# Kernel optimization log

Measured on AMD Instinct MI355X. Metric: run time of the kernel, lower is better.

The kernel has to match this reference:

```python
import jax, jax.numpy as jnp
import numpy as np
from jax import lax

V, EMB, ENH, DNH, ZD, K = 51, 64, 256, 256, 32, 512
B, T = 1024, 128


def gru_scan(xs, h0, Wih, Whh, bih, bhh, collect):
    """PyTorch-convention GRU. xs: [T,B,D], h0: [B,H]. Returns (ys or None, hT)."""
    def step(h, x):
        gi = x @ Wih.T + bih          # [B, 3H]
        gh = h @ Whh.T + bhh          # [B, 3H]
        ir, iz, inn = jnp.split(gi, 3, axis=-1)
        hr, hz, hn = jnp.split(gh, 3, axis=-1)
        r = jax.nn.sigmoid(ir + hr)
        zg = jax.nn.sigmoid(iz + hz)
        n = jnp.tanh(inn + r * hn)
        hnew = (1.0 - zg) * n + zg * h
        return hnew, (hnew if collect else None)
    hT, ys = lax.scan(step, h0, xs)
    return ys, hT


def setup_inputs() -> dict:
    key = jax.random.key(0)
    ks = jax.random.split(key, 24)
    w = lambda k, shape, s=0.1: (jax.random.normal(k, shape, jnp.float32) * s)
    inp = {
        "x": jax.random.randint(ks[0], (B, T), 0, V),
        "emb_enc": w(ks[1], (V, EMB)),
        "emb_dec": w(ks[2], (V, EMB)),
        # encoder bidirectional GRU (fwd + bwd directions)
        "Wih_f": w(ks[3], (3 * ENH, EMB)), "Whh_f": w(ks[4], (3 * ENH, ENH)),
        "bih_f": w(ks[5], (3 * ENH,)), "bhh_f": w(ks[6], (3 * ENH,)),
        "Wih_b": w(ks[7], (3 * ENH, EMB)), "Whh_b": w(ks[8], (3 * ENH, ENH)),
        "bih_b": w(ks[9], (3 * ENH,)), "bhh_b": w(ks[10], (3 * ENH,)),
        # down_to_z: Linear(2*ENC_NH -> Z_NH)
        "Wdown": w(ks[11], (ZD, 2 * ENH)), "bdown": w(ks[12], (ZD,)),
        # VQ codebook, uniform(-1/K, 1/K) as in source
        "codebook": jax.random.uniform(ks[13], (K, ZD), jnp.float32, -1.0 / K, 1.0 / K),
        # up_from_z: Linear(Z_NH -> DEC_NH)
        "Wup": w(ks[14], (DNH, ZD)), "bup": w(ks[15], (DNH,)),
        # decoder GRU: input = INPUT_EMB_DIM + Z_NH
        "Wih_d": w(ks[16], (3 * DNH, EMB + ZD)), "Whh_d": w(ks[17], (3 * DNH, DNH)),
        "bih_d": w(ks[18], (3 * DNH,)), "bhh_d": w(ks[19], (3 * DNH,)),
        # output projection Linear(DEC_NH -> VOCABSIZE)
        "Wout": w(ks[20], (V, DNH)), "bout": w(ks[21], (V,)),
    }
    return inp


def reference(x, emb_enc, emb_dec, Wih_f, Whh_f, bih_f, bhh_f,
              Wih_b, Whh_b, bih_b, bhh_b, Wdown, bdown, codebook,
              Wup, bup, Wih_d, Whh_d, bih_d, bhh_d, Wout, bout):
    sg = lax.stop_gradient
    Bsz, Tlen = x.shape

    # ---- Encoder: bidirectional GRU, keep final hidden of each direction ----
    e = emb_enc[x]                              # [B,T,EMB]
    xs = jnp.transpose(e, (1, 0, 2))            # [T,B,EMB]
    h0 = jnp.zeros((Bsz, ENH), e.dtype)
    _, hf = gru_scan(xs, h0, Wih_f, Whh_f, bih_f, bhh_f, collect=False)
    _, hb = gru_scan(xs[::-1], h0, Wih_b, Whh_b, bih_b, bhh_b, collect=False)
    out_h = jnp.concatenate([hf, hb], axis=-1)  # [B, 2*ENH]

    # ---- down to z ----
    z = out_h @ Wdown.T + bdown                 # [B, ZD]

    # ---- VQ quantizer ----
    d2 = (z ** 2).sum(-1, keepdims=True) + (codebook ** 2).sum(-1) - 2.0 * (z @ codebook.T)  # [B,K]
    idx = jnp.argmin(d2, axis=-1)               # [B]
    quantized = codebook[idx]                   # [B, ZD]
    commit = ((sg(quantized) - z) ** 2).mean(-1)
    embed_l = ((quantized - sg(z)) ** 2).mean(-1)
    qloss = 0.1 * commit + 0.1 * embed_l
    Q = jnp.sum(qloss)
    qz = z + sg(quantized - z)                  # straight-through [B, ZD]

    # ---- up to decoder hidden ----
    hidden = qz @ Wup.T + bup                   # [B, DNH]

    # ---- Decoder GRU over src, z concatenated at every step ----
    src, tgt = x[:, :-1], x[:, 1:]
    d = emb_dec[src]                            # [B,T-1,EMB]
    zrep = jnp.broadcast_to(qz[:, None, :], (Bsz, Tlen - 1, ZD))
    dec_in = jnp.concatenate([zrep, d], axis=-1)            # [B,T-1,EMB+ZD]
    ys, _ = gru_scan(jnp.transpose(dec_in, (1, 0, 2)), hidden,
                     Wih_d, Whh_d, bih_d, bhh_d, collect=True)  # [T-1,B,DNH]
    logits = jnp.transpose(ys, (1, 0, 2)) @ Wout.T + bout   # [B,T-1,V]

    # cross entropy, reduction='sum', ignore_index=0
    logp = jax.nn.log_softmax(logits, axis=-1)
    nll = -jnp.take_along_axis(logp, tgt[..., None], axis=-1).squeeze(-1)  # [B,T-1]
    mask = (tgt != 0)
    xloss = jnp.sum(nll * mask)
    nonpadded_tokens = jnp.sum(mask)
    pred_tokens = jnp.argmax(logits, axis=-1)

    return (xloss, nonpadded_tokens, pred_tokens, Q, idx[:, None])
```

## Files before the change

kernel.cpp:

```cpp
#include <hip/hip_runtime.h>
#include <cstdint>

typedef unsigned short u16;
typedef unsigned int u32;
typedef __attribute__((ext_vector_type(4))) int int4v;
typedef __attribute__((ext_vector_type(8))) short short8;
typedef __attribute__((ext_vector_type(4))) float f32x4;

#define XLOSS_OFF 0
#define NPAD_OFF  1
#define PRED_OFF  2
#define Q_OFF     130050
#define IDX_OFF   130051

__device__ __forceinline__ u16 f2b(float f){
  union { float f; unsigned int i; } c; c.f = f;
  unsigned int i = c.i;
  unsigned int r = (i + 0x7FFFu + ((i >> 16) & 1u)) >> 16;
  return (u16)r;
}

#define LOG2E 1.442695040889634f
__device__ __forceinline__ float fast_sigmoid(float x){
  return __builtin_amdgcn_rcpf(1.f + __builtin_amdgcn_exp2f(-LOG2E*x));
}
__device__ __forceinline__ float fast_tanh(float x){
  return 1.f - 2.f*__builtin_amdgcn_rcpf(1.f + __builtin_amdgcn_exp2f((2.f*LOG2E)*x));
}

__global__ __launch_bounds__(256) void k_prep_wo(
    const float* __restrict__ Wo, u16* __restrict__ oWo, float* __restrict__ dout){
  int idx = blockIdx.x*256 + threadIdx.x;
  if (idx == 0){ dout[XLOSS_OFF]=0.f; dout[NPAD_OFF]=0.f; dout[Q_OFF]=0.f; }
  int row = idx >> 8, k = idx & 255;
  oWo[idx] = (row < 51) ? f2b(Wo[row*256 + k]) : (u16)0;
}

__global__ __launch_bounds__(64) void k_prep_q(
    const float* __restrict__ Wf, const float* __restrict__ Wb, const float* __restrict__ Wd,
    signed char* __restrict__ qf, signed char* __restrict__ qb, signed char* __restrict__ qd,
    float* __restrict__ invf, float* __restrict__ invb, float* __restrict__ invd){
  const int row = blockIdx.x;
  const int mat = row / 768, r = row - mat*768;
  const float* W = (mat==0 ? Wf : (mat==1 ? Wb : Wd)) + (size_t)r*256;
  signed char* q = (mat==0 ? qf : (mat==1 ? qb : qd)) + (size_t)r*256;
  float* inv     = (mat==0 ? invf : (mat==1 ? invb : invd));
  const int lane = threadIdx.x;
  float4 v = *(const float4*)(W + lane*4);
  float m = fmaxf(fmaxf(fabsf(v.x),fabsf(v.y)), fmaxf(fabsf(v.z),fabsf(v.w)));
  #pragma unroll
  for (int off=32; off>0; off>>=1) m = fmaxf(m, __shfl_xor(m, off));
  m = fmaxf(m, 1e-20f);
  const float s = 127.f / m;
  int a0 = __float2int_rn(v.x*s), a1 = __float2int_rn(v.y*s);
  int a2 = __float2int_rn(v.z*s), a3 = __float2int_rn(v.w*s);
  u32 packed = (a0&255) | ((a1&255)<<8) | ((a2&255)<<16) | ((a3&255)<<24);
  *(u32*)(q + lane*4) = packed;
  if (lane == 0) inv[r] = m * (1.f/127.f);
}

__global__ __launch_bounds__(256) void k_prep_g(
    const float* __restrict__ emb_e, const float* __restrict__ emb_d,
    const float* __restrict__ Wih_f, const float* __restrict__ bih_f, const float* __restrict__ bhh_f,
    const float* __restrict__ Wih_b, const float* __restrict__ bih_b, const float* __restrict__ bhh_b,
    const float* __restrict__ Wih_d,
    float* __restrict__ Gf, float* __restrict__ Gb, float* __restrict__ Gd){
  int idx = blockIdx.x*256 + threadIdx.x;
  int tab = idx / 39168;
  int rem = idx - tab*39168;
  int v = rem / 768;
  int n = rem - v*768;
  float acc = 0.f;
  if (tab == 0){
    const float* e = emb_e + v*64; const float* w = Wih_f + n*64;
    for (int k=0;k<64;k++) acc += e[k]*w[k];
    acc += bih_f[n] + (n < 512 ? bhh_f[n] : 0.f);
    Gf[rem] = acc;
  } else if (tab == 1){
    const float* e = emb_e + v*64; const float* w = Wih_b + n*64;
    for (int k=0;k<64;k++) acc += e[k]*w[k];
    acc += bih_b[n] + (n < 512 ? bhh_b[n] : 0.f);
    Gb[rem] = acc;
  } else {
    const float* e = emb_d + v*64; const float* w = Wih_d + n*96 + 32;
    for (int k=0;k<64;k++) acc += e[k]*w[k];
    Gd[rem] = acc;
  }
}

template<int MODE>
__global__ __launch_bounds__(1024)
__attribute__((amdgpu_waves_per_eu(4, 4)))
void k_gru(
    const signed char* __restrict__ W0, const signed char* __restrict__ W1,
    const float* __restrict__ I0, const float* __restrict__ I1,
    const float* __restrict__ G0, const float* __restrict__ G1,
    const float* __restrict__ bhh0, const float* __restrict__ bhh1,
    const int* __restrict__ x,
    const float* __restrict__ zc, const float* __restrict__ h0g,
    float* __restrict__ out_h, u16* __restrict__ ys){
  const int tid = threadIdx.x;
  const int lane = tid & 63;
  const int wave = tid >> 6;
  const int l15 = lane & 15, lhi = lane >> 4;

  bool fwd = true; int gb;
  const signed char* W; const float* G; const float* bhh; const float* invS;
  if (MODE == 0){
    int bi = blockIdx.x;
    fwd = bi < 64; gb = fwd ? bi : bi - 64;
    W = fwd ? W0 : W1; G = fwd ? G0 : G1; bhh = fwd ? bhh0 : bhh1;
    invS = fwd ? I0 : I1;
  } else {
    gb = blockIdx.x; W = W0; G = G0; bhh = bhh0; invS = I0;
  }
  const int b0 = gb * 16;
  const int nT = (MODE == 0) ? 128 : 127;
  const float HS    = (MODE == 0) ? 127.f : 63.f;
  const float invHS = (MODE == 0) ? (1.f/127.f) : (1.f/63.f);

  __shared__ signed char hbf[2*4096];
  __shared__ int xsh[2048];
  __shared__ float zcs[(MODE==1) ? (16*768) : 4];

  const int c = wave*16 + l15;

  int4v wq0[4], wq1[4], wq2[4];
  {
    const signed char* p0 = W + (size_t)(c      )*256 + lhi*16;
    const signed char* p1 = W + (size_t)(c + 256)*256 + lhi*16;
    const signed char* p2 = W + (size_t)(c + 512)*256 + lhi*16;
    #pragma unroll
    for (int kt=0; kt<4; kt++){
      wq0[kt] = *(const int4v*)(p0 + kt*64);
      wq1[kt] = *(const int4v*)(p1 + kt*64);
      wq2[kt] = *(const int4v*)(p2 + kt*64);
    }
  }
  #pragma unroll
  for (int kt=0; kt<4; kt++){
    asm volatile("" : "+v"(wq0[kt]));
    asm volatile("" : "+v"(wq1[kt]));
    asm volatile("" : "+v"(wq2[kt]));
  }
  const float isr = invS[c]       * invHS;
  const float isz = invS[256 + c] * invHS;
  const float isn = invS[512 + c] * invHS;
  const float bnv = bhh[512 + c];

  for (int i = tid; i < 2048; i += 1024) xsh[i] = x[b0*128 + i];
  if (MODE == 1){
    for (int i = tid; i < 12288; i += 1024) zcs[i] = zc[(size_t)b0*768 + i];
  }

  float hreg[4];
  #pragma unroll
  for (int r=0;r<4;r++){
    const int m = 4*lhi + r;
    float hv = (MODE==0) ? 0.f : h0g[(size_t)(b0+m)*256 + c];
    hreg[r] = hv;
    int hq = __float2int_rn(fminf(fmaxf(hv*HS, -127.f), 127.f));
    hbf[m*256 + (c ^ ((m&15)<<4))] = (signed char)hq;
  }
  __syncthreads();

  int aoff[4];
  #pragma unroll
  for (int kt=0; kt<4; kt++)
    aoff[kt] = l15*256 + ((kt*64 + lhi*16) ^ (l15<<4));

  int cur = 0;
  for (int t=0; t<nT; ++t){
    const signed char* hb = hbf + (cur<<12);
    int4v af[4];
    #pragma unroll
    for (int kt=0; kt<4; kt++) af[kt] = *(const int4v*)(hb + aoff[kt]);

    int4v acc0 = {0,0,0,0}, acc1 = {0,0,0,0}, acc2 = {0,0,0,0};
    #pragma unroll
    for (int kt=0; kt<4; kt++){
      acc0 = __builtin_amdgcn_mfma_i32_16x16x64_i8(af[kt], wq0[kt], acc0, 0,0,0);
      acc1 = __builtin_amdgcn_mfma_i32_16x16x64_i8(af[kt], wq1[kt], acc1, 0,0,0);
      acc2 = __builtin_amdgcn_mfma_i32_16x16x64_i8(af[kt], wq2[kt], acc2, 0,0,0);
    }

    const int te = (MODE==0 && !fwd) ? (127 - t) : t;
    signed char* nbuf = hbf + ((cur^1)<<12);
    #pragma unroll
    for (int r=0;r<4;r++){
      const int m = 4*lhi + r;
      const int tok = xsh[(m<<7) + te];
      const float* Gp = G + (size_t)tok*768;
      float gr = Gp[c], gz = Gp[256 + c], gn = Gp[512 + c];
      if (MODE==1){
        const float* zp = &zcs[m*768];
        gr += zp[c]; gz += zp[256 + c]; gn += zp[512 + c];
      }
      float ghr = (float)acc0[r] * isr;
      float ghz = (float)acc1[r] * isz;
      float ghn = (float)acc2[r] * isn;
      float rg = fast_sigmoid(ghr + gr);
      float zg = fast_sigmoid(ghz + gz);
      float nn = fast_tanh(gn + rg*(ghn + bnv));
      float hv = nn + zg*(hreg[r] - nn);
      hreg[r] = hv;
      int hq = __float2int_rn(fminf(fmaxf(hv*HS, -127.f), 127.f));
      nbuf[m*256 + (c ^ ((m&15)<<4))] = (signed char)hq;
      if (MODE == 1){
        ys[((size_t)(b0+m)*127 + t)*256 + c] = f2b(hv);
      }
    }
    __syncthreads();
    cur ^= 1;
  }

  if (MODE == 0){
    #pragma unroll
    for (int r=0;r<4;r++){
      const int m = 4*lhi + r;
      out_h[(size_t)(b0+m)*512 + (fwd ? 0 : 256) + c] = hreg[r];
    }
  }
}

__global__ __launch_bounds__(64) void k_vq(
    const float* __restrict__ outH, const float* __restrict__ Wdown, const float* __restrict__ bdown,
    const float* __restrict__ cb, const float* __restrict__ Wup, const float* __restrict__ bup,
    const float* __restrict__ Wihd, const float* __restrict__ bihd, const float* __restrict__ bhhd,
    float* __restrict__ hidden, float* __restrict__ zc, float* __restrict__ dout){
  const int b = blockIdx.x;
  const int lane = threadIdx.x;
  __shared__ float oh[512];
  __shared__ float zsh[32];
  __shared__ float qsh[32];
  {
    const float* src = outH + (size_t)b*512 + lane*8;
    *(float4*)&oh[lane*8]   = *(const float4*)src;
    *(float4*)&oh[lane*8+4] = *(const float4*)(src+4);
  }
  __syncthreads();
  if (lane < 32){
    float acc = bdown[lane];
    const float* wr = Wdown + lane*512;
    for (int k=0;k<512;k++) acc += wr[k]*oh[k];
    zsh[lane] = acc;
  }
  __syncthreads();
  float bd = 3.4e38f; int bi = 0;
  for (int c8=0;c8<8;c8++){
    const int c = lane*8 + c8;
    const float* cr = cb + c*32;
    float d = 0.f;
    #pragma unroll
    for (int k=0;k<32;k++){ float df = zsh[k]-cr[k]; d += df*df; }
    if (d < bd){ bd = d; bi = c; }
  }
  #pragma unroll
  for (int offm=32; offm>0; offm>>=1){
    float od = __shfl_xor(bd, offm);
    int   oi = __shfl_xor(bi, offm);
    if (od < bd || (od == bd && oi < bi)){ bd = od; bi = oi; }
  }
  if (lane == 0){
    atomicAdd(&dout[Q_OFF], bd * (0.2f/32.f));
    dout[IDX_OFF + b] = (float)bi;
  }
  if (lane < 32) qsh[lane] = cb[(size_t)bi*32 + lane];
  __syncthreads();
  #pragma unroll
  for (int i=0;i<4;i++){
    const int o = lane*4 + i;
    float acc = bup[o];
    const float* wr = Wup + o*32;
    #pragma unroll
    for (int k=0;k<32;k++) acc += wr[k]*qsh[k];
    hidden[(size_t)b*256 + o] = acc;
  }
  #pragma unroll
  for (int i=0;i<12;i++){
    const int o = lane*12 + i;
    float acc = bihd[o] + (o < 512 ? bhhd[o] : 0.f);
    const float* wr = Wihd + (size_t)o*96;
    #pragma unroll
    for (int k=0;k<32;k++) acc += wr[k]*qsh[k];
    zc[(size_t)b*768 + o] = acc;
  }
}

__global__ __launch_bounds__(256) void k_out(
    const u16* __restrict__ ys, const u16* __restrict__ Wo,
    const float* __restrict__ bout, const int* __restrict__ x,
    float* __restrict__ dout){
  const int tid = threadIdx.x;
  const int w = tid >> 6, lane = tid & 63;
  const int l15 = lane & 15, lhi = lane >> 4;
  __shared__ float lg[4][32][66];
  const int rows0 = blockIdx.x*128 + w*32;
  const f32x4 fz = {0.f,0.f,0.f,0.f};
  #pragma unroll
  for (int mt=0; mt<2; mt++){
    const int rb = rows0 + mt*16;
    f32x4 acc[4];
    #pragma unroll
    for (int nt=0;nt<4;nt++) acc[nt] = fz;
    #pragma unroll
    for (int kt=0; kt<8; kt++){
      short8 a = *(const short8*)&ys[(size_t)(rb + l15)*256 + kt*32 + lhi*8];
      #pragma unroll
      for (int nt=0; nt<4; nt++){
        short8 bb = *(const short8*)&Wo[(size_t)(nt*16 + l15)*256 + kt*32 + lhi*8];
        acc[nt] = __builtin_amdgcn_mfma_f32_16x16x32_bf16(a, bb, acc[nt], 0, 0, 0);
      }
    }
    #pragma unroll
    for (int nt=0;nt<4;nt++){
      const int col = nt*16 + l15;
      const float bo = (col < 51) ? bout[col] : 0.f;
      #pragma unroll
      for (int r=0;r<4;r++){
        float v = (col < 51) ? (acc[nt][r] + bo) : -1e30f;
        lg[w][mt*16 + lhi*4 + r][col] = v;
      }
    }
  }
  __syncthreads();
  float xl = 0.f, ct = 0.f;
  if (lane < 32){
    const int grow = rows0 + lane;
    const float* Lr = &lg[w][lane][0];
    float m = Lr[0]; int am = 0;
    for (int i=1;i<51;i++){ float v = Lr[i]; if (v > m){ m = v; am = i; } }
    float s = 0.f;
    for (int i=0;i<51;i++) s += __expf(Lr[i] - m);
    const int bb = grow / 127;
    const int tt = grow - bb*127;
    const int tgt = x[bb*128 + tt + 1];
    const float nll = (m + __logf(s)) - Lr[tgt];
    const float mk = (tgt != 0) ? 1.f : 0.f;
    dout[PRED_OFF + grow] = (float)am;
    xl = nll * mk; ct = mk;
  }
  #pragma unroll
  for (int off=32; off>0; off>>=1){
    xl += __shfl_xor(xl, off);
    ct += __shfl_xor(ct, off);
  }
  if (lane == 0){
    atomicAdd(&dout[XLOSS_OFF], xl);
    atomicAdd(&dout[NPAD_OFF], ct);
  }
}

extern "C" void kernel_launch(void* const* d_in, const int* in_sizes, int n_in,
                              void* d_out, int out_size, void* d_ws, size_t ws_size,
                              hipStream_t stream){
  (void)in_sizes; (void)n_in; (void)out_size; (void)ws_size;
  const int*   x      = (const int*)  d_in[0];
  const float* emb_e  = (const float*)d_in[1];
  const float* emb_d  = (const float*)d_in[2];
  const float* Wih_f  = (const float*)d_in[3];
  const float* Whh_f  = (const float*)d_in[4];
  const float* bih_f  = (const float*)d_in[5];
  const float* bhh_f  = (const float*)d_in[6];
  const float* Wih_b  = (const float*)d_in[7];
  const float* Whh_b  = (const float*)d_in[8];
  const float* bih_b  = (const float*)d_in[9];
  const float* bhh_b  = (const float*)d_in[10];
  const float* Wdown  = (const float*)d_in[11];
  const float* bdown  = (const float*)d_in[12];
  const float* cbook  = (const float*)d_in[13];
  const float* Wup    = (const float*)d_in[14];
  const float* bup    = (const float*)d_in[15];
  const float* Wih_d  = (const float*)d_in[16];
  const float* Whh_d  = (const float*)d_in[17];
  const float* bih_d  = (const float*)d_in[18];
  const float* bhh_d  = (const float*)d_in[19];
  const float* Wout   = (const float*)d_in[20];
  const float* bout   = (const float*)d_in[21];
  float* dout = (float*)d_out;

  char* ws = (char*)d_ws;
  size_t off = 0;
  auto nxt = [&](size_t bytes)->char*{
    char* r = ws + off;
    off += (bytes + 255) & ~(size_t)255;
    return r;
  };
  signed char* Wq_f = (signed char*)nxt((size_t)196608);
  signed char* Wq_b = (signed char*)nxt((size_t)196608);
  signed char* Wq_d = (signed char*)nxt((size_t)196608);
  float* invF = (float*)nxt((size_t)768*4);
  float* invB = (float*)nxt((size_t)768*4);
  float* invD = (float*)nxt((size_t)768*4);
  float* Gf    = (float*)nxt((size_t)39168*4);
  float* Gb    = (float*)nxt((size_t)39168*4);
  float* Gd    = (float*)nxt((size_t)39168*4);
  u16*   Wo_bf = (u16*)  nxt((size_t)16384*2);
  float* outH  = (float*)nxt((size_t)524288*4);
  float* hid   = (float*)nxt((size_t)262144*4);
  float* zcw   = (float*)nxt((size_t)786432*4);
  u16*   ysb   = (u16*)  nxt((size_t)33292288*2);

  hipLaunchKernelGGL(k_prep_wo, dim3(64), dim3(256), 0, stream, Wout, Wo_bf, dout);
  hipLaunchKernelGGL(k_prep_q, dim3(2304), dim3(64), 0, stream,
                     Whh_f, Whh_b, Whh_d, Wq_f, Wq_b, Wq_d, invF, invB, invD);
  hipLaunchKernelGGL(k_prep_g, dim3(459), dim3(256), 0, stream,
                     emb_e, emb_d, Wih_f, bih_f, bhh_f, Wih_b, bih_b, bhh_b, Wih_d,
                     Gf, Gb, Gd);
  hipLaunchKernelGGL((k_gru<0>), dim3(128), dim3(1024), 0, stream,
                     Wq_f, Wq_b, invF, invB, Gf, Gb, bhh_f, bhh_b, x,
                     (const float*)nullptr, (const float*)nullptr, outH, (u16*)nullptr);
  hipLaunchKernelGGL(k_vq, dim3(1024), dim3(64), 0, stream,
                     outH, Wdown, bdown, cbook, Wup, bup, Wih_d, bih_d, bhh_d,
                     hid, zcw, dout);
  hipLaunchKernelGGL((k_gru<1>), dim3(64), dim3(1024), 0, stream,
                     Wq_d, (const signed char*)nullptr, invD, (const float*)nullptr,
                     Gd, (const float*)nullptr, bhh_d, (const float*)nullptr, x,
                     zcw, hid, (float*)nullptr, ysb);
  hipLaunchKernelGGL(k_out, dim3(1016), dim3(256), 0, stream,
                     ysb, Wo_bf, bout, x, dout);
}
```

Measured before the change: 578.1 us.

## Stage r/z recurrent weights in LDS instead of registers in GRU kernel

The r and z gate int8 recurrent weights move from per-thread registers into a swizzled 128KB LDS buffer that is loaded once per block. Only the n-gate weights stay register-resident. Each step now reads the r/z weight fragments from LDS alongside the hidden state, which frees VGPRs but adds LDS traffic to every recurrence step. The decoder's per-batch z contribution is read directly from global memory instead of staged in LDS, and dynamic shared memory of 144KB is requested for both GRU launches.

```diff
diff --git a/kernel.cpp b/kernel.cpp
--- a/kernel.cpp
+++ b/kernel.cpp
@@ -12,6 +12,8 @@
 #define PRED_OFF  2
 #define Q_OFF     130050
 #define IDX_OFF   130051
+
+#define GRU_LDS_BYTES 147456
 
 __device__ __forceinline__ u16 f2b(float f){
   union { float f; unsigned int i; } c; c.f = f;
@@ -99,6 +101,11 @@
     const int* __restrict__ x,
     const float* __restrict__ zc, const float* __restrict__ h0g,
     float* __restrict__ out_h, u16* __restrict__ ys){
+  extern __shared__ char smem[];
+  signed char* wlds = (signed char*)smem;
+  signed char* hbf  = (signed char*)(smem + 131072);
+  int*         xsh  = (int*)(smem + 139264);
+
   const int tid = threadIdx.x;
   const int lane = tid & 63;
   const int wave = tid >> 6;
@@ -119,39 +126,32 @@
   const float HS    = (MODE == 0) ? 127.f : 63.f;
   const float invHS = (MODE == 0) ? (1.f/127.f) : (1.f/63.f);
 
-  __shared__ signed char hbf[2*4096];
-  __shared__ int xsh[2048];
-  __shared__ float zcs[(MODE==1) ? (16*768) : 4];
-
   const int c = wave*16 + l15;
 
-  int4v wq0[4], wq1[4], wq2[4];
+  #pragma unroll
+  for (int it=0; it<8; ++it){
+    int i = tid + it*1024;
+    int row = i >> 4;
+    int ck  = (i & 15) << 4;
+    int4v v = *(const int4v*)(W + (size_t)row*256 + ck);
+    *(int4v*)(wlds + row*256 + (ck ^ ((row&15)<<4))) = v;
+  }
+
+  int4v wq2[4];
   {
-    const signed char* p0 = W + (size_t)(c      )*256 + lhi*16;
-    const signed char* p1 = W + (size_t)(c + 256)*256 + lhi*16;
     const signed char* p2 = W + (size_t)(c + 512)*256 + lhi*16;
     #pragma unroll
-    for (int kt=0; kt<4; kt++){
-      wq0[kt] = *(const int4v*)(p0 + kt*64);
-      wq1[kt] = *(const int4v*)(p1 + kt*64);
-      wq2[kt] = *(const int4v*)(p2 + kt*64);
-    }
-  }
-  #pragma unroll
-  for (int kt=0; kt<4; kt++){
-    asm volatile("" : "+v"(wq0[kt]));
-    asm volatile("" : "+v"(wq1[kt]));
-    asm volatile("" : "+v"(wq2[kt]));
-  }
+    for (int kt=0; kt<4; kt++) wq2[kt] = *(const int4v*)(p2 + kt*64);
+  }
+  #pragma unroll
+  for (int kt=0; kt<4; kt++){ asm volatile("" : "+v"(wq2[kt])); }
+
   const float isr = invS[c]       * invHS;
   const float isz = invS[256 + c] * invHS;
   const float isn = invS[512 + c] * invHS;
   const float bnv = bhh[512 + c];
 
   for (int i = tid; i < 2048; i += 1024) xsh[i] = x[b0*128 + i];
-  if (MODE == 1){
-    for (int i = tid; i < 12288; i += 1024) zcs[i] = zc[(size_t)b0*768 + i];
-  }
 
   float hreg[4];
   #pragma unroll
@@ -164,24 +164,25 @@
   }
   __syncthreads();
 
-  int aoff[4];
-  #pragma unroll
-  for (int kt=0; kt<4; kt++)
-    aoff[kt] = l15*256 + ((kt*64 + lhi*16) ^ (l15<<4));
+  int koff[4];
+  #pragma unroll
+  for (int kt=0; kt<4; kt++) koff[kt] = (kt*64 + lhi*16) ^ (l15<<4);
+  const int arow = l15 << 8;
+  const int wrow = (wave*16 + l15) << 8;
 
   int cur = 0;
   for (int t=0; t<nT; ++t){
     const signed char* hb = hbf + (cur<<12);
-    int4v af[4];
-    #pragma unroll
-    for (int kt=0; kt<4; kt++) af[kt] = *(const int4v*)(hb + aoff[kt]);
 
     int4v acc0 = {0,0,0,0}, acc1 = {0,0,0,0}, acc2 = {0,0,0,0};
     #pragma unroll
     for (int kt=0; kt<4; kt++){
-      acc0 = __builtin_amdgcn_mfma_i32_16x16x64_i8(af[kt], wq0[kt], acc0, 0,0,0);
-      acc1 = __builtin_amdgcn_mfma_i32_16x16x64_i8(af[kt], wq1[kt], acc1, 0,0,0);
-      acc2 = __builtin_amdgcn_mfma_i32_16x16x64_i8(af[kt], wq2[kt], acc2, 0,0,0);
+      int4v af = *(const int4v*)(hb + arow + koff[kt]);
+      int4v wr = *(const int4v*)(wlds + wrow + koff[kt]);
+      int4v wz = *(const int4v*)(wlds + wrow + 65536 + koff[kt]);
+      acc0 = __builtin_amdgcn_mfma_i32_16x16x64_i8(af, wr, acc0, 0,0,0);
+      acc1 = __builtin_amdgcn_mfma_i32_16x16x64_i8(af, wz, acc1, 0,0,0);
+      acc2 = __builtin_amdgcn_mfma_i32_16x16x64_i8(af, wq2[kt], acc2, 0,0,0);
     }
 
     const int te = (MODE==0 && !fwd) ? (127 - t) : t;
@@ -193,8 +194,8 @@
       const float* Gp = G + (size_t)tok*768;
       float gr = Gp[c], gz = Gp[256 + c], gn = Gp[512 + c];
       if (MODE==1){
-        const float* zp = &zcs[m*768];
-        gr += zp[c]; gz += zp[256 + c]; gn += zp[512 + c];
+        const float* zp = zc + (size_t)(b0+m)*768 + c;
+        gr += zp[0]; gz += zp[256]; gn += zp[512];
       }
       float ghr = (float)acc0[r] * isr;
       float ghz = (float)acc1[r] * isz;
@@ -401,19 +402,24 @@
   float* zcw   = (float*)nxt((size_t)786432*4);
   u16*   ysb   = (u16*)  nxt((size_t)33292288*2);
 
+  hipFuncSetAttribute((const void*)&k_gru<0>,
+                      hipFuncAttributeMaxDynamicSharedMemorySize, GRU_LDS_BYTES);
+  hipFuncSetAttribute((const void*)&k_gru<1>,
+                      hipFuncAttributeMaxDynamicSharedMemorySize, GRU_LDS_BYTES);
+
   hipLaunchKernelGGL(k_prep_wo, dim3(64), dim3(256), 0, stream, Wout, Wo_bf, dout);
   hipLaunchKernelGGL(k_prep_q, dim3(2304), dim3(64), 0, stream,
                      Whh_f, Whh_b, Whh_d, Wq_f, Wq_b, Wq_d, invF, invB, invD);
   hipLaunchKernelGGL(k_prep_g, dim3(459), dim3(256), 0, stream,
                      emb_e, emb_d, Wih_f, bih_f, bhh_f, Wih_b, bih_b, bhh_b, Wih_d,
                      Gf, Gb, Gd);
-  hipLaunchKernelGGL((k_gru<0>), dim3(128), dim3(1024), 0, stream,
+  hipLaunchKernelGGL((k_gru<0>), dim3(128), dim3(1024), GRU_LDS_BYTES, stream,
                      Wq_f, Wq_b, invF, invB, Gf, Gb, bhh_f, bhh_b, x,
                      (const float*)nullptr, (const float*)nullptr, outH, (u16*)nullptr);
   hipLaunchKernelGGL(k_vq, dim3(1024), dim3(64), 0, stream,
                      outH, Wdown, bdown, cbook, Wup, bup, Wih_d, bih_d, bhh_d,
                      hid, zcw, dout);
-  hipLaunchKernelGGL((k_gru<1>), dim3(64), dim3(1024), 0, stream,
+  hipLaunchKernelGGL((k_gru<1>), dim3(64), dim3(1024), GRU_LDS_BYTES, stream,
                      Wq_d, (const signed char*)nullptr, invD, (const float*)nullptr,
                      Gd, (const float*)nullptr, bhh_d, (const float*)nullptr, x,
                      zcw, hid, (float*)nullptr, ysb);
```

Result: slower. 628.4 us (+8.7%).

## Split GRU recurrence into 8-row blocks of 4 waves with register-held weights

Applied to the files above, without the earlier changes.

The recurrent GRU kernel goes from 1024-thread blocks over 16 batch rows to 256-thread blocks over 8 batch rows. This doubles the grid to 256 blocks for the encoder and 128 for the decoder, so more CUs run the serial time loop. Each wave now keeps 64 columns of all three gate weights in registers and issues 48 int8 MFMAs per step, and only half the lanes do the gate math because the M dimension is half used. Gate inputs are prefetched before the MFMAs, z-conditioning is held in registers, and decoder outputs are staged in shared memory for 16-byte coalesced stores at the cost of an extra barrier per step.

```diff
diff --git a/kernel.cpp b/kernel.cpp
--- a/kernel.cpp
+++ b/kernel.cpp
@@ -5,6 +5,7 @@
 typedef unsigned int u32;
 typedef __attribute__((ext_vector_type(4))) int int4v;
 typedef __attribute__((ext_vector_type(8))) short short8;
+typedef __attribute__((ext_vector_type(8))) unsigned short u16x8;
 typedef __attribute__((ext_vector_type(4))) float f32x4;
 
 #define XLOSS_OFF 0
@@ -89,8 +90,8 @@
 }
 
 template<int MODE>
-__global__ __launch_bounds__(1024)
-__attribute__((amdgpu_waves_per_eu(4, 4)))
+__global__ __launch_bounds__(256)
+__attribute__((amdgpu_waves_per_eu(1, 1)))
 void k_gru(
     const signed char* __restrict__ W0, const signed char* __restrict__ W1,
     const float* __restrict__ I0, const float* __restrict__ I1,
@@ -99,6 +100,10 @@
     const int* __restrict__ x,
     const float* __restrict__ zc, const float* __restrict__ h0g,
     float* __restrict__ out_h, u16* __restrict__ ys){
+  __shared__ signed char hbf[2*4096];
+  __shared__ int xsh[1024];
+  __shared__ u16 ysh[(MODE==1) ? 2048 : 4];
+
   const int tid = threadIdx.x;
   const int lane = tid & 63;
   const int wave = tid >> 6;
@@ -108,59 +113,80 @@
   const signed char* W; const float* G; const float* bhh; const float* invS;
   if (MODE == 0){
     int bi = blockIdx.x;
-    fwd = bi < 64; gb = fwd ? bi : bi - 64;
+    fwd = bi < 128; gb = fwd ? bi : bi - 128;
     W = fwd ? W0 : W1; G = fwd ? G0 : G1; bhh = fwd ? bhh0 : bhh1;
     invS = fwd ? I0 : I1;
   } else {
     gb = blockIdx.x; W = W0; G = G0; bhh = bhh0; invS = I0;
   }
-  const int b0 = gb * 16;
+  const int b0 = gb * 8;
   const int nT = (MODE == 0) ? 128 : 127;
   const float HS    = (MODE == 0) ? 127.f : 63.f;
   const float invHS = (MODE == 0) ? (1.f/127.f) : (1.f/63.f);
 
-  __shared__ signed char hbf[2*4096];
-  __shared__ int xsh[2048];
-  __shared__ float zcs[(MODE==1) ? (16*768) : 4];
-
-  const int c = wave*16 + l15;
-
-  int4v wq0[4], wq1[4], wq2[4];
-  {
-    const signed char* p0 = W + (size_t)(c      )*256 + lhi*16;
-    const signed char* p1 = W + (size_t)(c + 256)*256 + lhi*16;
-    const signed char* p2 = W + (size_t)(c + 512)*256 + lhi*16;
-    #pragma unroll
-    for (int kt=0; kt<4; kt++){
-      wq0[kt] = *(const int4v*)(p0 + kt*64);
-      wq1[kt] = *(const int4v*)(p1 + kt*64);
-      wq2[kt] = *(const int4v*)(p2 + kt*64);
-    }
-  }
-  #pragma unroll
-  for (int kt=0; kt<4; kt++){
-    asm volatile("" : "+v"(wq0[kt]));
-    asm volatile("" : "+v"(wq1[kt]));
-    asm volatile("" : "+v"(wq2[kt]));
-  }
-  const float isr = invS[c]       * invHS;
-  const float isz = invS[256 + c] * invHS;
-  const float isn = invS[512 + c] * invHS;
-  const float bnv = bhh[512 + c];
-
-  for (int i = tid; i < 2048; i += 1024) xsh[i] = x[b0*128 + i];
-  if (MODE == 1){
-    for (int i = tid; i < 12288; i += 1024) zcs[i] = zc[(size_t)b0*768 + i];
-  }
-
-  float hreg[4];
-  #pragma unroll
-  for (int r=0;r<4;r++){
-    const int m = 4*lhi + r;
-    float hv = (MODE==0) ? 0.f : h0g[(size_t)(b0+m)*256 + c];
-    hreg[r] = hv;
-    int hq = __float2int_rn(fminf(fmaxf(hv*HS, -127.f), 127.f));
-    hbf[m*256 + (c ^ ((m&15)<<4))] = (signed char)hq;
+  int4v wq[3][4][4];
+  #pragma unroll
+  for (int g=0; g<3; g++){
+    #pragma unroll
+    for (int ct=0; ct<4; ct++){
+      const signed char* p = W + (size_t)(g*256 + wave*64 + ct*16 + l15)*256 + lhi*16;
+      #pragma unroll
+      for (int kt=0; kt<4; kt++)
+        wq[g][ct][kt] = *(const int4v*)(p + kt*64);
+    }
+  }
+  #pragma unroll
+  for (int g=0; g<3; g++)
+    #pragma unroll
+    for (int ct=0; ct<4; ct++)
+      #pragma unroll
+      for (int kt=0; kt<4; kt++){ asm volatile("" : "+v"(wq[g][ct][kt])); }
+
+  float is_[3][4], bn_[4];
+  #pragma unroll
+  for (int ct=0; ct<4; ct++){
+    const int col = wave*64 + ct*16 + l15;
+    is_[0][ct] = invS[col]       * invHS;
+    is_[1][ct] = invS[256 + col] * invHS;
+    is_[2][ct] = invS[512 + col] * invHS;
+    bn_[ct]    = bhh[512 + col];
+  }
+
+  float zv[3][16];
+  if (MODE == 1 && lhi < 2){
+    #pragma unroll
+    for (int ct=0; ct<4; ct++){
+      const int col = wave*64 + ct*16 + l15;
+      #pragma unroll
+      for (int r=0; r<4; r++){
+        const int m = 4*lhi + r;
+        const float* zp = zc + (size_t)(b0+m)*768 + col;
+        zv[0][ct*4+r] = zp[0];
+        zv[1][ct*4+r] = zp[256];
+        zv[2][ct*4+r] = zp[512];
+      }
+    }
+  }
+
+  for (int i = tid; i < 1024; i += 256) xsh[i] = x[b0*128 + i];
+  for (int i = tid*4; i < 8192; i += 1024) *(int*)&hbf[i] = 0;
+
+  float hreg[16];
+  #pragma unroll
+  for (int i=0;i<16;i++) hreg[i] = 0.f;
+  if (MODE == 1 && lhi < 2){
+    #pragma unroll
+    for (int ct=0; ct<4; ct++){
+      const int col = wave*64 + ct*16 + l15;
+      #pragma unroll
+      for (int r=0; r<4; r++){
+        const int m = 4*lhi + r;
+        float hv = h0g[(size_t)(b0+m)*256 + col];
+        hreg[ct*4+r] = hv;
+        int hq = __float2int_rn(fminf(fmaxf(hv*HS, -127.f), 127.f));
+        hbf[m*256 + (col ^ ((m&15)<<4))] = (signed char)hq;
+      }
+    }
   }
   __syncthreads();
 
@@ -176,49 +202,82 @@
     #pragma unroll
     for (int kt=0; kt<4; kt++) af[kt] = *(const int4v*)(hb + aoff[kt]);
 
-    int4v acc0 = {0,0,0,0}, acc1 = {0,0,0,0}, acc2 = {0,0,0,0};
-    #pragma unroll
-    for (int kt=0; kt<4; kt++){
-      acc0 = __builtin_amdgcn_mfma_i32_16x16x64_i8(af[kt], wq0[kt], acc0, 0,0,0);
-      acc1 = __builtin_amdgcn_mfma_i32_16x16x64_i8(af[kt], wq1[kt], acc1, 0,0,0);
-      acc2 = __builtin_amdgcn_mfma_i32_16x16x64_i8(af[kt], wq2[kt], acc2, 0,0,0);
-    }
-
     const int te = (MODE==0 && !fwd) ? (127 - t) : t;
+    float gv[3][16];
+    if (lhi < 2){
+      #pragma unroll
+      for (int ct=0; ct<4; ct++){
+        const int col = wave*64 + ct*16 + l15;
+        #pragma unroll
+        for (int r=0; r<4; r++){
+          const int m = 4*lhi + r;
+          const int tok = xsh[(m<<7) + te];
+          const float* Gp = G + (size_t)tok*768 + col;
+          gv[0][ct*4+r] = Gp[0];
+          gv[1][ct*4+r] = Gp[256];
+          gv[2][ct*4+r] = Gp[512];
+        }
+      }
+    }
+
+    int4v acc[3][4];
+    #pragma unroll
+    for (int g=0; g<3; g++)
+      #pragma unroll
+      for (int ct=0; ct<4; ct++) acc[g][ct] = (int4v){0,0,0,0};
+    #pragma unroll
+    for (int kt=0; kt<4; kt++)
+      #pragma unroll
+      for (int g=0; g<3; g++)
+        #pragma unroll
+        for (int ct=0; ct<4; ct++)
+          acc[g][ct] = __builtin_amdgcn_mfma_i32_16x16x64_i8(af[kt], wq[g][ct][kt], acc[g][ct], 0,0,0);
+
     signed char* nbuf = hbf + ((cur^1)<<12);
-    #pragma unroll
-    for (int r=0;r<4;r++){
-      const int m = 4*lhi + r;
-      const int tok = xsh[(m<<7) + te];
-      const float* Gp = G + (size_t)tok*768;
-      float gr = Gp[c], gz = Gp[256 + c], gn = Gp[512 + c];
-      if (MODE==1){
-        const float* zp = &zcs[m*768];
-        gr += zp[c]; gz += zp[256 + c]; gn += zp[512 + c];
-      }
-      float ghr = (float)acc0[r] * isr;
-      float ghz = (float)acc1[r] * isz;
-      float ghn = (float)acc2[r] * isn;
-      float rg = fast_sigmoid(ghr + gr);
-      float zg = fast_sigmoid(ghz + gz);
-      float nn = fast_tanh(gn + rg*(ghn + bnv));
-      float hv = nn + zg*(hreg[r] - nn);
-      hreg[r] = hv;
-      int hq = __float2int_rn(fminf(fmaxf(hv*HS, -127.f), 127.f));
-      nbuf[m*256 + (c ^ ((m&15)<<4))] = (signed char)hq;
-      if (MODE == 1){
-        ys[((size_t)(b0+m)*127 + t)*256 + c] = f2b(hv);
+    if (lhi < 2){
+      #pragma unroll
+      for (int ct=0; ct<4; ct++){
+        const int col = wave*64 + ct*16 + l15;
+        #pragma unroll
+        for (int r=0; r<4; r++){
+          const int idx = ct*4 + r;
+          const int m = 4*lhi + r;
+          float gr = gv[0][idx], gz = gv[1][idx], gn = gv[2][idx];
+          if (MODE == 1){ gr += zv[0][idx]; gz += zv[1][idx]; gn += zv[2][idx]; }
+          float ghr = (float)acc[0][ct][r] * is_[0][ct];
+          float ghz = (float)acc[1][ct][r] * is_[1][ct];
+          float ghn = (float)acc[2][ct][r] * is_[2][ct];
+          float rg = fast_sigmoid(ghr + gr);
+          float zg = fast_sigmoid(ghz + gz);
+          float nn = fast_tanh(gn + rg*(ghn + bn_[ct]));
+          float hv = nn + zg*(hreg[idx] - nn);
+          hreg[idx] = hv;
+          int hq = __float2int_rn(fminf(fmaxf(hv*HS, -127.f), 127.f));
+          nbuf[m*256 + (col ^ ((m&15)<<4))] = (signed char)hq;
+          if (MODE == 1) ysh[m*256 + col] = f2b(hv);
+        }
       }
     }
     __syncthreads();
+    if (MODE == 1){
+      const int row = tid >> 5;
+      const int c8  = (tid & 31) * 8;
+      u16x8 v = *(const u16x8*)&ysh[row*256 + c8];
+      *(u16x8*)&ys[((size_t)(b0+row)*127 + t)*256 + c8] = v;
+      __syncthreads();
+    }
     cur ^= 1;
   }
 
-  if (MODE == 0){
-    #pragma unroll
-    for (int r=0;r<4;r++){
-      const int m = 4*lhi + r;
-      out_h[(size_t)(b0+m)*512 + (fwd ? 0 : 256) + c] = hreg[r];
+  if (MODE == 0 && lhi < 2){
+    #pragma unroll
+    for (int ct=0; ct<4; ct++){
+      const int col = wave*64 + ct*16 + l15;
+      #pragma unroll
+      for (int r=0; r<4; r++){
+        const int m = 4*lhi + r;
+        out_h[(size_t)(b0+m)*512 + (fwd ? 0 : 256) + col] = hreg[ct*4+r];
+      }
     }
   }
 }
@@ -395,7 +454,7 @@
   float* Gf    = (float*)nxt((size_t)39168*4);
   float* Gb    = (float*)nxt((size_t)39168*4);
   float* Gd    = (float*)nxt((size_t)39168*4);
-  u16*   Wo_bf = (u16*)  nxt((size_t)16384*2);
+  u16*   Wo_bf = (u16*) nxt((size_t)16384*2);
   float* outH  = (float*)nxt((size_t)524288*4);
   float* hid   = (float*)nxt((size_t)262144*4);
   float* zcw   = (float*)nxt((size_t)786432*4);
@@ -407,13 +466,13 @@
   hipLaunchKernelGGL(k_prep_g, dim3(459), dim3(256), 0, stream,
                      emb_e, emb_d, Wih_f, bih_f, bhh_f, Wih_b, bih_b, bhh_b, Wih_d,
                      Gf, Gb, Gd);
-  hipLaunchKernelGGL((k_gru<0>), dim3(128), dim3(1024), 0, stream,
+  hipLaunchKernelGGL((k_gru<0>), dim3(256), dim3(256), 0, stream,
                      Wq_f, Wq_b, invF, invB, Gf, Gb, bhh_f, bhh_b, x,
                      (const float*)nullptr, (const float*)nullptr, outH, (u16*)nullptr);
   hipLaunchKernelGGL(k_vq, dim3(1024), dim3(64), 0, stream,
                      outH, Wdown, bdown, cbook, Wup, bup, Wih_d, bih_d, bhh_d,
                      hid, zcw, dout);
-  hipLaunchKernelGGL((k_gru<1>), dim3(64), dim3(1024), 0, stream,
+  hipLaunchKernelGGL((k_gru<1>), dim3(128), dim3(256), 0, stream,
                      Wq_d, (const signed char*)nullptr, invD, (const float*)nullptr,
                      Gd, (const float*)nullptr, bhh_d, (const float*)nullptr, x,
                      zcw, hid, (float*)nullptr, ysb);
```

New measurement: 816.7 us. +41.3%, slower.

## Halve GRU block size, give each wave two 16-column tiles per gate

Applied to the files above, without the earlier changes.

The recurrent GRU kernels now run with 512 threads instead of 1024. Each wave owns 32 hidden columns (two 16-wide MFMA tiles per gate, six accumulators), so it keeps twice as many int8 weight registers. The per-step cost moves from more waves doing fewer MFMAs to fewer waves doing more, which cuts barrier participants and shared A-fragment reloads. The decoder's z-contribution is now read straight from global memory instead of being staged in shared memory, which trades LDS for global or L2 loads on every step. Register pressure rises and the waves_per_eu hint drops to 2.

```diff
diff --git a/kernel.cpp b/kernel.cpp
--- a/kernel.cpp
+++ b/kernel.cpp
@@ -89,8 +89,8 @@
 }
 
 template<int MODE>
-__global__ __launch_bounds__(1024)
-__attribute__((amdgpu_waves_per_eu(4, 4)))
+__global__ __launch_bounds__(512)
+__attribute__((amdgpu_waves_per_eu(2, 2)))
 void k_gru(
     const signed char* __restrict__ W0, const signed char* __restrict__ W1,
     const float* __restrict__ I0, const float* __restrict__ I1,
@@ -99,6 +99,9 @@
     const int* __restrict__ x,
     const float* __restrict__ zc, const float* __restrict__ h0g,
     float* __restrict__ out_h, u16* __restrict__ ys){
+  __shared__ signed char hbf[2*4096];
+  __shared__ int xsh[2048];
+
   const int tid = threadIdx.x;
   const int lane = tid & 63;
   const int wave = tid >> 6;
@@ -119,48 +122,52 @@
   const float HS    = (MODE == 0) ? 127.f : 63.f;
   const float invHS = (MODE == 0) ? (1.f/127.f) : (1.f/63.f);
 
-  __shared__ signed char hbf[2*4096];
-  __shared__ int xsh[2048];
-  __shared__ float zcs[(MODE==1) ? (16*768) : 4];
-
-  const int c = wave*16 + l15;
-
-  int4v wq0[4], wq1[4], wq2[4];
-  {
-    const signed char* p0 = W + (size_t)(c      )*256 + lhi*16;
-    const signed char* p1 = W + (size_t)(c + 256)*256 + lhi*16;
-    const signed char* p2 = W + (size_t)(c + 512)*256 + lhi*16;
-    #pragma unroll
-    for (int kt=0; kt<4; kt++){
-      wq0[kt] = *(const int4v*)(p0 + kt*64);
-      wq1[kt] = *(const int4v*)(p1 + kt*64);
-      wq2[kt] = *(const int4v*)(p2 + kt*64);
+  const int ca  = wave*32 + l15;
+  const int cb2 = ca + 16;
+
+  int4v wq[6][4];
+  #pragma unroll
+  for (int g=0; g<3; g++){
+    #pragma unroll
+    for (int hh=0; hh<2; hh++){
+      const signed char* p = W + (size_t)(g*256 + wave*32 + hh*16 + l15)*256 + lhi*16;
+      #pragma unroll
+      for (int kt=0; kt<4; kt++)
+        wq[g*2+hh][kt] = *(const int4v*)(p + kt*64);
     }
   }
   #pragma unroll
   for (int kt=0; kt<4; kt++){
-    asm volatile("" : "+v"(wq0[kt]));
-    asm volatile("" : "+v"(wq1[kt]));
-    asm volatile("" : "+v"(wq2[kt]));
-  }
-  const float isr = invS[c]       * invHS;
-  const float isz = invS[256 + c] * invHS;
-  const float isn = invS[512 + c] * invHS;
-  const float bnv = bhh[512 + c];
-
-  for (int i = tid; i < 2048; i += 1024) xsh[i] = x[b0*128 + i];
-  if (MODE == 1){
-    for (int i = tid; i < 12288; i += 1024) zcs[i] = zc[(size_t)b0*768 + i];
-  }
-
-  float hreg[4];
+    asm volatile("" : "+v"(wq[0][kt]));
+    asm volatile("" : "+v"(wq[1][kt]));
+    asm volatile("" : "+v"(wq[2][kt]));
+    asm volatile("" : "+v"(wq[3][kt]));
+    asm volatile("" : "+v"(wq[4][kt]));
+    asm volatile("" : "+v"(wq[5][kt]));
+  }
+  const float is0 = invS[ca]        * invHS;
+  const float is1 = invS[cb2]       * invHS;
+  const float is2 = invS[256 + ca]  * invHS;
+  const float is3 = invS[256 + cb2] * invHS;
+  const float is4 = invS[512 + ca]  * invHS;
+  const float is5 = invS[512 + cb2] * invHS;
+  const float bn0 = bhh[512 + ca];
+  const float bn1 = bhh[512 + cb2];
+
+  for (int i = tid; i < 2048; i += 512) xsh[i] = x[b0*128 + i];
+
+  float hr0[4], hr1[4];
   #pragma unroll
   for (int r=0;r<4;r++){
     const int m = 4*lhi + r;
-    float hv = (MODE==0) ? 0.f : h0g[(size_t)(b0+m)*256 + c];
-    hreg[r] = hv;
-    int hq = __float2int_rn(fminf(fmaxf(hv*HS, -127.f), 127.f));
-    hbf[m*256 + (c ^ ((m&15)<<4))] = (signed char)hq;
+    const int sw = (m&15)<<4;
+    float v0 = (MODE==0) ? 0.f : h0g[(size_t)(b0+m)*256 + ca];
+    float v1 = (MODE==0) ? 0.f : h0g[(size_t)(b0+m)*256 + cb2];
+    hr0[r] = v0; hr1[r] = v1;
+    int q0 = __float2int_rn(fminf(fmaxf(v0*HS, -127.f), 127.f));
+    int q1 = __float2int_rn(fminf(fmaxf(v1*HS, -127.f), 127.f));
+    hbf[m*256 + (ca  ^ sw)] = (signed char)q0;
+    hbf[m*256 + (cb2 ^ sw)] = (signed char)q1;
   }
   __syncthreads();
 
@@ -176,13 +183,14 @@
     #pragma unroll
     for (int kt=0; kt<4; kt++) af[kt] = *(const int4v*)(hb + aoff[kt]);
 
-    int4v acc0 = {0,0,0,0}, acc1 = {0,0,0,0}, acc2 = {0,0,0,0};
-    #pragma unroll
-    for (int kt=0; kt<4; kt++){
-      acc0 = __builtin_amdgcn_mfma_i32_16x16x64_i8(af[kt], wq0[kt], acc0, 0,0,0);
-      acc1 = __builtin_amdgcn_mfma_i32_16x16x64_i8(af[kt], wq1[kt], acc1, 0,0,0);
-      acc2 = __builtin_amdgcn_mfma_i32_16x16x64_i8(af[kt], wq2[kt], acc2, 0,0,0);
-    }
+    int4v acc[6];
+    #pragma unroll
+    for (int j=0;j<6;j++) acc[j] = (int4v){0,0,0,0};
+    #pragma unroll
+    for (int kt=0; kt<4; kt++)
+      #pragma unroll
+      for (int j=0;j<6;j++)
+        acc[j] = __builtin_amdgcn_mfma_i32_16x16x64_i8(af[kt], wq[j][kt], acc[j], 0,0,0);
 
     const int te = (MODE==0 && !fwd) ? (127 - t) : t;
     signed char* nbuf = hbf + ((cur^1)<<12);
@@ -191,23 +199,33 @@
       const int m = 4*lhi + r;
       const int tok = xsh[(m<<7) + te];
       const float* Gp = G + (size_t)tok*768;
-      float gr = Gp[c], gz = Gp[256 + c], gn = Gp[512 + c];
+      float gr0 = Gp[ca],  gz0 = Gp[256+ca],  gn0 = Gp[512+ca];
+      float gr1 = Gp[cb2], gz1 = Gp[256+cb2], gn1 = Gp[512+cb2];
       if (MODE==1){
-        const float* zp = &zcs[m*768];
-        gr += zp[c]; gz += zp[256 + c]; gn += zp[512 + c];
+        const float* zp = zc + (size_t)(b0+m)*768;
+        gr0 += zp[ca];  gz0 += zp[256+ca];  gn0 += zp[512+ca];
+        gr1 += zp[cb2]; gz1 += zp[256+cb2]; gn1 += zp[512+cb2];
       }
-      float ghr = (float)acc0[r] * isr;
-      float ghz = (float)acc1[r] * isz;
-      float ghn = (float)acc2[r] * isn;
-      float rg = fast_sigmoid(ghr + gr);
-      float zg = fast_sigmoid(ghz + gz);
-      float nn = fast_tanh(gn + rg*(ghn + bnv));
-      float hv = nn + zg*(hreg[r] - nn);
-      hreg[r] = hv;
-      int hq = __float2int_rn(fminf(fmaxf(hv*HS, -127.f), 127.f));
-      nbuf[m*256 + (c ^ ((m&15)<<4))] = (signed char)hq;
-      if (MODE == 1){
-        ys[((size_t)(b0+m)*127 + t)*256 + c] = f2b(hv);
+      const int sw = (m&15)<<4;
+      {
+        float rg = fast_sigmoid((float)acc[0][r]*is0 + gr0);
+        float zg = fast_sigmoid((float)acc[2][r]*is2 + gz0);
+        float nn = fast_tanh(gn0 + rg*((float)acc[4][r]*is4 + bn0));
+        float hv = nn + zg*(hr0[r] - nn);
+        hr0[r] = hv;
+        int hq = __float2int_rn(fminf(fmaxf(hv*HS, -127.f), 127.f));
+        nbuf[m*256 + (ca ^ sw)] = (signed char)hq;
+        if (MODE == 1) ys[((size_t)(b0+m)*127 + t)*256 + ca] = f2b(hv);
+      }
+      {
+        float rg = fast_sigmoid((float)acc[1][r]*is1 + gr1);
+        float zg = fast_sigmoid((float)acc[3][r]*is3 + gz1);
+        float nn = fast_tanh(gn1 + rg*((float)acc[5][r]*is5 + bn1));
+        float hv = nn + zg*(hr1[r] - nn);
+        hr1[r] = hv;
+        int hq = __float2int_rn(fminf(fmaxf(hv*HS, -127.f), 127.f));
+        nbuf[m*256 + (cb2 ^ sw)] = (signed char)hq;
+        if (MODE == 1) ys[((size_t)(b0+m)*127 + t)*256 + cb2] = f2b(hv);
       }
     }
     __syncthreads();
@@ -218,7 +236,9 @@
     #pragma unroll
     for (int r=0;r<4;r++){
       const int m = 4*lhi + r;
-      out_h[(size_t)(b0+m)*512 + (fwd ? 0 : 256) + c] = hreg[r];
+      float* dst = out_h + (size_t)(b0+m)*512 + (fwd ? 0 : 256);
+      dst[ca]  = hr0[r];
+      dst[cb2] = hr1[r];
     }
   }
 }
@@ -395,7 +415,7 @@
   float* Gf    = (float*)nxt((size_t)39168*4);
   float* Gb    = (float*)nxt((size_t)39168*4);
   float* Gd    = (float*)nxt((size_t)39168*4);
-  u16*   Wo_bf = (u16*)  nxt((size_t)16384*2);
+  u16*   Wo_bf = (u16*) nxt((size_t)16384*2);
   float* outH  = (float*)nxt((size_t)524288*4);
   float* hid   = (float*)nxt((size_t)262144*4);
   float* zcw   = (float*)nxt((size_t)786432*4);
@@ -407,13 +427,13 @@
   hipLaunchKernelGGL(k_prep_g, dim3(459), dim3(256), 0, stream,
                      emb_e, emb_d, Wih_f, bih_f, bhh_f, Wih_b, bih_b, bhh_b, Wih_d,
                      Gf, Gb, Gd);
-  hipLaunchKernelGGL((k_gru<0>), dim3(128), dim3(1024), 0, stream,
+  hipLaunchKernelGGL((k_gru<0>), dim3(128), dim3(512), 0, stream,
                      Wq_f, Wq_b, invF, invB, Gf, Gb, bhh_f, bhh_b, x,
                      (const float*)nullptr, (const float*)nullptr, outH, (u16*)nullptr);
   hipLaunchKernelGGL(k_vq, dim3(1024), dim3(64), 0, stream,
                      outH, Wdown, bdown, cbook, Wup, bup, Wih_d, bih_d, bhh_d,
                      hid, zcw, dout);
-  hipLaunchKernelGGL((k_gru<1>), dim3(64), dim3(1024), 0, stream,
+  hipLaunchKernelGGL((k_gru<1>), dim3(64), dim3(512), 0, stream,
                      Wq_d, (const signed char*)nullptr, invD, (const float*)nullptr,
                      Gd, (const float*)nullptr, bhh_d, (const float*)nullptr, x,
                      zcw, hid, (float*)nullptr, ysb);
```

Result: slower. 601.3 us (+4.0%).
